# Optimization experiments

Hardware: AMD Instinct MI355X
Metric: run time of the kernel (lower is better)

## Reference

```python
import jax, jax.numpy as jnp
import numpy as np

B, N, D_V, D_MODEL, D_FF, N_HEADS = 32, 64, 6, 128, 512, 8


def _ln(x, g, b):
    m = x.mean(-1, keepdims=True)
    v = ((x - m) ** 2).mean(-1, keepdims=True)
    return (x - m) / jnp.sqrt(v + 1e-5) * g + b


def _mha(q_in, k_in, v_in, mask, Wq, Wk, Wv, Wo):
    # mask: (b, Lq, Lk) bool, True = attend
    b, Lq, D = q_in.shape
    H, dh = N_HEADS, D_MODEL // N_HEADS
    q = (q_in @ Wq).reshape(b, Lq, H, dh)
    k = (k_in @ Wk).reshape(b, k_in.shape[1], H, dh)
    v = (v_in @ Wv).reshape(b, v_in.shape[1], H, dh)
    s = jnp.einsum('bqhd,bkhd->bhqk', q, k) / (dh ** 0.5)
    s = jnp.where(mask[:, None, :, :], s, -1e9)
    o = jnp.einsum('bhqk,bkhd->bqhd', jax.nn.softmax(s, axis=-1), v).reshape(b, Lq, D)
    return o @ Wo


def setup_inputs() -> dict:
    key = jax.random.key(0)
    ks = jax.random.split(key, 40)
    def p(i, shape, scale=0.05):
        return jax.random.normal(ks[i], shape, dtype=jnp.float32) * scale
    nm = jax.random.randint(ks[1], (B, N, N), 0, 2, dtype=jnp.int32)
    nm = nm.at[:, jnp.arange(N), jnp.arange(N)].set(1)  # self always a neighbor
    inp = {
        'agent_infos': jax.random.normal(ks[0], (B, N, N, D_V), dtype=jnp.float32),
        'neighbor_masks': nm,
        'padding_mask': jnp.ones((B, N), dtype=jnp.int32),
        'is_from_my_env': jnp.ones((B,), dtype=jnp.int32),
        # src_embed
        'W_emb': p(2, (D_V, D_MODEL)), 'b_emb': jnp.zeros((D_MODEL,), jnp.float32),
        # encoder layer (self-attn + FFN, post-LN)
        'Wq': p(3, (D_MODEL, D_MODEL)), 'Wk': p(4, (D_MODEL, D_MODEL)),
        'Wv': p(5, (D_MODEL, D_MODEL)), 'Wo': p(6, (D_MODEL, D_MODEL)),
        'ln1_g': jnp.ones((D_MODEL,), jnp.float32), 'ln1_b': jnp.zeros((D_MODEL,), jnp.float32),
        'W1': p(7, (D_MODEL, D_FF)), 'b1': jnp.zeros((D_FF,), jnp.float32),
        'W2': p(8, (D_FF, D_MODEL)), 'b2': jnp.zeros((D_MODEL,), jnp.float32),
        'ln2_g': jnp.ones((D_MODEL,), jnp.float32), 'ln2_b': jnp.zeros((D_MODEL,), jnp.float32),
        # decoder layer (cross-attn + FFN, post-LN)
        'Uq': p(9, (D_MODEL, D_MODEL)), 'Uk': p(10, (D_MODEL, D_MODEL)),
        'Uv': p(11, (D_MODEL, D_MODEL)), 'Uo': p(12, (D_MODEL, D_MODEL)),
        'ln3_g': jnp.ones((D_MODEL,), jnp.float32), 'ln3_b': jnp.zeros((D_MODEL,), jnp.float32),
        'W3': p(13, (D_MODEL, D_FF)), 'b3': jnp.zeros((D_FF,), jnp.float32),
        'W4': p(14, (D_FF, D_MODEL)), 'b4': jnp.zeros((D_MODEL,), jnp.float32),
        'ln4_g': jnp.ones((D_MODEL,), jnp.float32), 'ln4_b': jnp.zeros((D_MODEL,), jnp.float32),
        # generator (single-head query/key scorer)
        'Wg_q': p(15, (D_MODEL, D_MODEL)), 'Wg_k': p(16, (D_MODEL, D_MODEL)),
    }
    return inp


def reference(agent_infos, neighbor_masks, padding_mask, is_from_my_env,
              W_emb, b_emb, Wq, Wk, Wv, Wo, ln1_g, ln1_b, W1, b1, W2, b2, ln2_g, ln2_b,
              Uq, Uk, Uv, Uo, ln3_g, ln3_b, W3, b3, W4, b4, ln4_g, ln4_b, Wg_q, Wg_k):
    # Fold the per-agent python loop of the original into the batch dim: BN = B * N.
    src = agent_infos.reshape(B * N, N, D_V)
    neigh = neighbor_masks.reshape(B * N, N) != 0           # True = neighbor (attendable)
    x = src @ W_emb + b_emb                                 # (BN, N, D)
    src_mask = neigh[:, :, None] & neigh[:, None, :]        # (BN, N, N)
    x = _ln(x + _mha(x, x, x, src_mask, Wq, Wk, Wv, Wo), ln1_g, ln1_b)
    x = _ln(x + (jax.nn.relu(x @ W1 + b1) @ W2 + b2), ln2_g, ln2_b)
    # context vector -- faithful to the original get_context_vector (which sums rows
    # where pad_tokens==True, i.e. NON-neighbors, and divides by the neighbor count)
    pad = (~neigh)[:, :, None].astype(x.dtype)
    cnt = neigh.sum(axis=1).reshape(-1, 1, 1).astype(x.dtype)
    h_c = (x * pad).sum(axis=1, keepdims=True) / cnt        # (BN, 1, D)
    stm = neigh[:, None, :]                                 # src_tgt_mask (BN, 1, N)
    y = _ln(h_c + _mha(h_c, x, x, stm, Uq, Uk, Uv, Uo), ln3_g, ln3_b)
    y = _ln(y + (jax.nn.relu(y @ W3 + b3) @ W4 + b4), ln4_g, ln4_b)
    logits = jnp.einsum('bqd,bkd->bqk', y @ Wg_q, x @ Wg_k) / (D_MODEL ** 0.5)
    probs = jnp.where(stm, jax.nn.sigmoid(logits), 0.0)[:, 0, :]   # (BN, N)
    att_scores = probs.reshape(B, N, N)
    num_agents = padding_mask.sum(axis=1).astype(x.dtype).reshape(B, 1, 1)
    avg_h_c_N = h_c.reshape(B, N, D_MODEL).sum(axis=1, keepdims=True) / num_agents
    return att_scores, avg_h_c_N
```

## Files before the change

### kernel.cpp

```cpp
#include <hip/hip_runtime.h>
#include <hip/hip_bf16.h>
#include <math.h>

#define ITEMS 2048
#define SEQ   64
#define DM    128
#define DFF   512
#define ATT_OFF 131072

typedef unsigned short u16;
typedef __attribute__((ext_vector_type(4))) unsigned short ushort4v;
typedef __attribute__((ext_vector_type(8))) short short8v;
typedef __attribute__((ext_vector_type(4))) float float4v;

#define MFMA16(a,b,c) __builtin_amdgcn_mfma_f32_16x16x32_bf16(a,b,c,0,0,0)

#define XST 136
#define OST 136
#define QST 56
#define PST 76
#define VST 72

#define XS_B   0
#define OB_B   17408
#define QH_B   34816
#define KH_B   41984
#define VT_B   49152
#define P_B    34816
#define WALL_B 34816
#define SALL_B 38912
#define PALL_B 40960
#define TALL_B 43008
#define FF_B   38912
#define W4P_B  40960
#define HC_B   17408
#define QV_B   17920
#define OV_B   18432
#define YV_B   18944
#define Y2_B   19456
#define GW_B   19968
#define NF_B   51456
#define PF_B   51712
#define CNT_B  51968
#define NA_B   51972
#define NB_B   51976
#define ARENA_SZ 51984

__device__ __forceinline__ u16 f2b(float f){
  union { float f; unsigned u; } v; v.f = f;
  unsigned r = (v.u + 0x7fffu + ((v.u >> 16) & 1u)) >> 16;
  return (u16)r;
}
__device__ __forceinline__ float b2f(u16 h){
  union { unsigned u; float f; } v; v.u = ((unsigned)h) << 16;
  return v.f;
}
__device__ __forceinline__ float wsum(float v){
  #pragma unroll
  for (int off = 1; off < 64; off <<= 1) v += __shfl_xor(v, off);
  return v;
}
__device__ __forceinline__ void ln_vec(float* v, const float* g, const float* b, int lane){
  float v0 = v[lane], v1 = v[lane+64];
  float m  = wsum(v0+v1) * (1.f/128.f);
  float d0 = v0-m, d1 = v1-m;
  float var = wsum(d0*d0+d1*d1) * (1.f/128.f);
  float inv = rsqrtf(var + 1e-5f);
  v[lane]    = d0*inv*g[lane]    + b[lane];
  v[lane+64] = d1*inv*g[lane+64] + b[lane+64];
}

__global__ void prep_all(const float* __restrict__ Wq, const float* __restrict__ Wk,
                         const float* __restrict__ Wv, const float* __restrict__ Wo,
                         const float* __restrict__ Uk, const float* __restrict__ Uv,
                         const float* __restrict__ W1, const float* __restrict__ W2,
                         u16* __restrict__ wts){
  int idx = blockIdx.x*256 + threadIdx.x;
  if (idx >= 229376) return;
  if (idx < 98304){
    int wsel = idx >> 14, r = idx & 16383;
    const float* tab[6] = {Wq,Wk,Wv,Wo,Uk,Uv};
    int o = r >> 7, i = r & 127;
    wts[idx] = f2b(tab[wsel][i*128 + o]);
  } else if (idx < 163840){
    int r = idx - 98304;
    int o = r >> 7, i = r & 127;
    wts[idx] = f2b(W1[i*512 + o]);
  } else {
    int r = idx - 163840;
    int o = r >> 9, i = r & 511;
    wts[idx] = f2b(W2[i*128 + o]);
  }
}

__global__ void init_avg(float* __restrict__ out){
  out[ATT_OFF + blockIdx.x*256 + threadIdx.x] = 0.f;
}

__global__ __launch_bounds__(256, 3) void vicsek_fused(
    const float* __restrict__ agent_infos,
    const int*   __restrict__ nmask,
    const int*   __restrict__ pmask,
    const u16*   __restrict__ wts,
    const float* __restrict__ W_emb, const float* __restrict__ b_emb,
    const float* __restrict__ ln1g,  const float* __restrict__ ln1b,
    const float* __restrict__ b1,    const float* __restrict__ b2,
    const float* __restrict__ ln2g,  const float* __restrict__ ln2b,
    const float* __restrict__ Uq,    const float* __restrict__ Uo,
    const float* __restrict__ ln3g,  const float* __restrict__ ln3b,
    const float* __restrict__ W3,    const float* __restrict__ b3,
    const float* __restrict__ W4,    const float* __restrict__ b4,
    const float* __restrict__ ln4g,  const float* __restrict__ ln4b,
    const float* __restrict__ Wgq,   const float* __restrict__ Wgk,
    float* __restrict__ out)
{
  __shared__ __align__(16) char arena[ARENA_SZ];
  u16* Xs = (u16*)(arena + XS_B);
  u16* Ob = (u16*)(arena + OB_B);
  u16* Qh = (u16*)(arena + QH_B);
  u16* Kh = (u16*)(arena + KH_B);
  u16* VT = (u16*)(arena + VT_B);
  u16* Pl = (u16*)(arena + P_B);
  float* neighf = (float*)(arena + NF_B);
  float* padf   = (float*)(arena + PF_B);
  float* cnt_s  = (float*)(arena + CNT_B);
  float* na_s   = (float*)(arena + NA_B);
  unsigned long long* nb_s = (unsigned long long*)(arena + NB_B);

  const int item = blockIdx.x;
  const int tid  = threadIdx.x;
  const int lane = tid & 63;
  const int w    = tid >> 6;
  const int row0 = w*16;
  const int arow = lane & 15;
  const int akg  = lane >> 4;

  const u16* WqT = wts;          const u16* WkT = wts + 16384;
  const u16* WvT = wts + 32768;  const u16* WoT = wts + 49152;
  const u16* UkT = wts + 65536;  const u16* UvT = wts + 81920;
  const u16* W1T = wts + 98304;  const u16* W2T = wts + 163840;

  if (w == 0){
    int m = nmask[item*SEQ + lane];
    neighf[lane] = m ? 1.f : 0.f;
    padf[lane]   = m ? 0.f : 1.f;
    float c = wsum(m ? 1.f : 0.f);
    unsigned long long bb = __ballot(m != 0);
    if (lane == 0){ cnt_s[0] = c; nb_s[0] = bb; }
  }
  if (w == 1){
    float na = wsum((float)pmask[(item>>6)*SEQ + lane]);
    if (lane == 0) na_s[0] = na;
  }

  const float* src = agent_infos + (size_t)item*SEQ*6;
  for (int e = tid; e < SEQ*DM; e += 256){
    int r = e >> 7, c = e & 127;
    float a = b_emb[c];
    #pragma unroll
    for (int k = 0; k < 6; k++) a += src[r*6+k]*W_emb[k*DM+c];
    Xs[r*XST + c] = f2b(a);
  }
  __syncthreads();

  const unsigned long long nbits = nb_s[0];

  short8v aX[4];
  #pragma unroll
  for (int k = 0; k < 4; k++) aX[k] = *(const short8v*)(Xs + (row0+arow)*XST + k*32 + akg*8);

  for (int h = 0; h < 8; h++){
    __syncthreads();
    for (int idx = tid; idx < 1024; idx += 256){
      int r = idx >> 4, c2 = idx & 15;
      Qh[r*QST + 16 + c2] = 0;
      Kh[r*QST + 16 + c2] = 0;
    }
    {
      const u16* wq = WqT + (h*16+arow)*128 + akg*8;
      const u16* wk = WkT + (h*16+arow)*128 + akg*8;
      const u16* wv = WvT + (h*16+arow)*128 + akg*8;
      float4v cq = {0,0,0,0}, ck = {0,0,0,0}, cv = {0,0,0,0};
      #pragma unroll
      for (int k = 0; k < 4; k++){
        short8v bqf = *(const short8v*)(wq + k*32);
        short8v bkf = *(const short8v*)(wk + k*32);
        short8v bvf = *(const short8v*)(wv + k*32);
        cq = MFMA16(aX[k], bqf, cq);
        ck = MFMA16(aX[k], bkf, ck);
        cv = MFMA16(bvf, aX[k], cv);
      }
      #pragma unroll
      for (int i = 0; i < 4; i++){
        Qh[(row0+akg*4+i)*QST + arow] = f2b(cq[i]);
        Kh[(row0+akg*4+i)*QST + arow] = f2b(ck[i]);
        VT[(akg*4+i)*VST + row0 + arow] = f2b(cv[i]);
      }
    }
    __syncthreads();
    short8v bq = *(const short8v*)(Qh + (row0+arow)*QST + akg*8);
    float4v st[4];
    #pragma unroll
    for (int kb = 0; kb < 4; kb++){
      short8v akf = *(const short8v*)(Kh + (kb*16+arow)*QST + akg*8);
      float4v z = {0,0,0,0};
      st[kb] = MFMA16(akf, bq, z);
    }
    bool qok = (nbits >> (row0+arow)) & 1ull;
    float pr[16]; float mx = -3.0e38f;
    #pragma unroll
    for (int kb = 0; kb < 4; kb++)
      #pragma unroll
      for (int i = 0; i < 4; i++){
        int key = kb*16 + akg*4 + i;
        float s = st[kb][i]*0.25f;
        if (!qok || !((nbits>>key)&1ull)) s = -1.0e9f;
        pr[kb*4+i] = s; mx = fmaxf(mx, s);
      }
    mx = fmaxf(mx, __shfl_xor(mx,16)); mx = fmaxf(mx, __shfl_xor(mx,32));
    float sum = 0.f;
    #pragma unroll
    for (int z = 0; z < 16; z++){ pr[z] = __expf(pr[z]-mx); sum += pr[z]; }
    sum += __shfl_xor(sum,16); sum += __shfl_xor(sum,32);
    float inv = 1.f/sum;
    #pragma unroll
    for (int kb = 0; kb < 4; kb++)
      #pragma unroll
      for (int i = 0; i < 4; i++)
        Pl[(kb*16+akg*4+i)*PST + row0 + arow] = f2b(pr[kb*4+i]*inv);
    float4v ot = {0,0,0,0};
    #pragma unroll
    for (int c2 = 0; c2 < 2; c2++){
      short8v avf = *(const short8v*)(VT + arow*VST + c2*32 + akg*8);
      short8v bp;
      #pragma unroll
      for (int j = 0; j < 8; j++) bp[j] = (short)Pl[(c2*32+akg*8+j)*PST + row0 + arow];
      ot = MFMA16(avf, bp, ot);
    }
    ushort4v ov4;
    #pragma unroll
    for (int i = 0; i < 4; i++) ov4[i] = f2b(ot[i]);
    *(ushort4v*)(Ob + (row0+arow)*OST + h*16 + akg*4) = ov4;
  }

  {
    float4v accW[8];
    #pragma unroll
    for (int t = 0; t < 8; t++)
      #pragma unroll
      for (int i = 0; i < 4; i++)
        accW[t][i] = b2f(Xs[(row0+akg*4+i)*XST + t*16 + arow]);
    short8v aO[4];
    #pragma unroll
    for (int k = 0; k < 4; k++) aO[k] = *(const short8v*)(Ob + (row0+arow)*OST + k*32 + akg*8);
    #pragma unroll
    for (int k = 0; k < 4; k++)
      #pragma unroll
      for (int t = 0; t < 8; t++)
        accW[t] = MFMA16(aO[k], *(const short8v*)(WoT + (t*16+arow)*128 + k*32 + akg*8), accW[t]);
    float g8[8], bb8[8];
    #pragma unroll
    for (int t = 0; t < 8; t++){ g8[t] = ln1g[t*16+arow]; bb8[t] = ln1b[t*16+arow]; }
    #pragma unroll
    for (int i = 0; i < 4; i++){
      float sm = 0.f;
      #pragma unroll
      for (int t = 0; t < 8; t++) sm += accW[t][i];
      sm += __shfl_xor(sm,1); sm += __shfl_xor(sm,2); sm += __shfl_xor(sm,4); sm += __shfl_xor(sm,8);
      float mean = sm*(1.f/128.f);
      float vs = 0.f;
      #pragma unroll
      for (int t = 0; t < 8; t++){ float d = accW[t][i]-mean; vs += d*d; }
      vs += __shfl_xor(vs,1); vs += __shfl_xor(vs,2); vs += __shfl_xor(vs,4); vs += __shfl_xor(vs,8);
      float inv = rsqrtf(vs*(1.f/128.f) + 1e-5f);
      #pragma unroll
      for (int t = 0; t < 8; t++)
        Xs[(row0+akg*4+i)*XST + t*16 + arow] = f2b((accW[t][i]-mean)*inv*g8[t] + bb8[t]);
    }
  }
  #pragma unroll
  for (int k = 0; k < 4; k++) aX[k] = *(const short8v*)(Xs + (row0+arow)*XST + k*32 + akg*8);

  {
    float4v accY[8];
    #pragma unroll
    for (int t = 0; t < 8; t++){
      float bb = b2[t*16 + arow];
      #pragma unroll
      for (int i = 0; i < 4; i++)
        accY[t][i] = bb + b2f(Xs[(row0+akg*4+i)*XST + t*16 + arow]);
    }
    for (int c = 0; c < 4; c++){
      #pragma unroll
      for (int t = 0; t < 8; t++){
        float bb = b1[c*128 + t*16 + arow];
        float4v acc = {bb,bb,bb,bb};
        #pragma unroll
        for (int k = 0; k < 4; k++)
          acc = MFMA16(aX[k], *(const short8v*)(W1T + (c*128+t*16+arow)*128 + k*32 + akg*8), acc);
        #pragma unroll
        for (int i = 0; i < 4; i++)
          Ob[(row0+akg*4+i)*OST + t*16 + arow] = f2b(fmaxf(acc[i], 0.f));
      }
      #pragma unroll
      for (int k = 0; k < 4; k++){
        short8v aH = *(const short8v*)(Ob + (row0+arow)*OST + k*32 + akg*8);
        #pragma unroll
        for (int t = 0; t < 8; t++)
          accY[t] = MFMA16(aH, *(const short8v*)(W2T + (t*16+arow)*512 + c*128 + k*32 + akg*8), accY[t]);
      }
    }
    float g8[8], bb8[8];
    #pragma unroll
    for (int t = 0; t < 8; t++){ g8[t] = ln2g[t*16+arow]; bb8[t] = ln2b[t*16+arow]; }
    #pragma unroll
    for (int i = 0; i < 4; i++){
      float sm = 0.f;
      #pragma unroll
      for (int t = 0; t < 8; t++) sm += accY[t][i];
      sm += __shfl_xor(sm,1); sm += __shfl_xor(sm,2); sm += __shfl_xor(sm,4); sm += __shfl_xor(sm,8);
      float mean = sm*(1.f/128.f);
      float vs = 0.f;
      #pragma unroll
      for (int t = 0; t < 8; t++){ float d = accY[t][i]-mean; vs += d*d; }
      vs += __shfl_xor(vs,1); vs += __shfl_xor(vs,2); vs += __shfl_xor(vs,4); vs += __shfl_xor(vs,8);
      float inv = rsqrtf(vs*(1.f/128.f) + 1e-5f);
      #pragma unroll
      for (int t = 0; t < 8; t++)
        Xs[(row0+akg*4+i)*XST + t*16 + arow] = f2b((accY[t][i]-mean)*inv*g8[t] + bb8[t]);
    }
  }
  __syncthreads();

  float* hc   = (float*)(arena + HC_B);
  float* qv   = (float*)(arena + QV_B);
  float* ov   = (float*)(arena + OV_B);
  float* yv   = (float*)(arena + YV_B);
  float* y2   = (float*)(arena + Y2_B);
  float* gw   = (float*)(arena + GW_B);
  float* wall = (float*)(arena + WALL_B);
  float* sall = (float*)(arena + SALL_B);
  float* pall = (float*)(arena + PALL_B);
  float* tall = (float*)(arena + TALL_B);
  float* ff   = (float*)(arena + FF_B);
  float* w4p  = (float*)(arena + W4P_B);

  if (tid < DM){
    float a = 0.f;
    for (int r = 0; r < SEQ; r++) a += b2f(Xs[r*XST + tid]) * padf[r];
    a /= cnt_s[0];
    hc[tid] = a;
    atomicAdd(&out[ATT_OFF + (item>>6)*DM + tid], a/na_s[0]);
  }
  __syncthreads();

  if (tid < DM){
    float a = 0.f;
    #pragma unroll 8
    for (int e = 0; e < DM; e++) a += hc[e]*Uq[e*DM + tid];
    qv[tid] = a;
  }
  __syncthreads();
  if (tid < DM){
    #pragma unroll
    for (int h = 0; h < 8; h++){
      float a = 0.f;
      #pragma unroll
      for (int d = 0; d < 16; d++) a += b2f(UkT[(h*16+d)*128 + tid]) * qv[h*16+d];
      wall[h*128 + tid] = a;
    }
  }
  __syncthreads();
  for (int idx = tid; idx < 512; idx += 256){
    int h = idx >> 6, j = idx & 63;
    const short8v* xr = (const short8v*)(Xs + j*XST);
    const float* wv_ = wall + h*128;
    float a = 0.f;
    #pragma unroll
    for (int c8 = 0; c8 < 16; c8++){
      short8v v = xr[c8];
      #pragma unroll
      for (int q = 0; q < 8; q++) a += b2f((u16)v[q]) * wv_[c8*8+q];
    }
    sall[idx] = a*0.25f;
  }
  __syncthreads();
  for (int hh = w; hh < 8; hh += 4){
    float s = sall[hh*64 + lane];
    if (!((nbits>>lane)&1ull)) s = -1.0e9f;
    float mxx = s;
    #pragma unroll
    for (int off = 1; off < 64; off <<= 1) mxx = fmaxf(mxx, __shfl_xor(mxx, off));
    float p = __expf(s - mxx);
    float su = wsum(p);
    pall[hh*64 + lane] = p/su;
  }
  __syncthreads();
  for (int idx = tid; idx < 1024; idx += 256){
    int h = idx >> 7, c = idx & 127;
    float a = 0.f;
    for (int j = 0; j < SEQ; j++) a += pall[h*64+j] * b2f(Xs[j*XST + c]);
    tall[idx] = a;
  }
  __syncthreads();
  if (tid < DM){
    const short8v* ur = (const short8v*)(UvT + tid*128);
    const float* th = tall + (tid>>4)*128;
    float a = 0.f;
    #pragma unroll
    for (int c8 = 0; c8 < 16; c8++){
      short8v v = ur[c8];
      #pragma unroll
      for (int q = 0; q < 8; q++) a += b2f((u16)v[q]) * th[c8*8+q];
    }
    ov[tid] = a;
  }
  __syncthreads();
  if (tid < DM){
    float a = 0.f;
    #pragma unroll 8
    for (int e = 0; e < DM; e++) a += ov[e]*Uo[e*DM + tid];
    yv[tid] = hc[tid] + a;
  }
  __syncthreads();
  if (w == 0) ln_vec(yv, ln3g, ln3b, lane);
  __syncthreads();

  for (int j = tid; j < DFF; j += 256){
    float a = b3[j];
    #pragma unroll 8
    for (int e = 0; e < DM; e++) a += yv[e]*W3[e*DFF + j];
    ff[j] = fmaxf(a, 0.f);
  }
  __syncthreads();
  {
    int o = tid & 127, half = tid >> 7;
    float a = 0.f;
    #pragma unroll 8
    for (int j = half*256; j < half*256+256; j++) a += ff[j]*W4[j*DM + o];
    w4p[tid] = a;
  }
  __syncthreads();
  if (tid < DM) y2[tid] = b4[tid] + yv[tid] + w4p[tid] + w4p[tid+128];
  __syncthreads();
  if (w == 0) ln_vec(y2, ln4g, ln4b, lane);
  __syncthreads();

  if (tid < DM){
    float a = 0.f;
    #pragma unroll 8
    for (int e = 0; e < DM; e++) a += y2[e]*Wgq[e*DM + tid];
    qv[tid] = a;
  }
  __syncthreads();
  if (tid < DM){
    const float4* wr = (const float4*)(Wgk + tid*DM);
    float a = 0.f;
    #pragma unroll
    for (int c4 = 0; c4 < 32; c4++){
      float4 v = wr[c4];
      a += v.x*qv[c4*4] + v.y*qv[c4*4+1] + v.z*qv[c4*4+2] + v.w*qv[c4*4+3];
    }
    gw[tid] = a;
  }
  __syncthreads();
  if (tid < SEQ){
    const short8v* xr = (const short8v*)(Xs + tid*XST);
    float a = 0.f;
    #pragma unroll
    for (int c8 = 0; c8 < 16; c8++){
      short8v v = xr[c8];
      #pragma unroll
      for (int q = 0; q < 8; q++) a += b2f((u16)v[q]) * gw[c8*8+q];
    }
    a *= 0.08838834764831845f;
    out[(size_t)item*SEQ + tid] = ((nbits>>tid)&1ull) ? (1.f/(1.f+__expf(-a))) : 0.f;
  }
}

extern "C" void kernel_launch(void* const* d_in, const int* in_sizes, int n_in,
                              void* d_out, int out_size, void* d_ws, size_t ws_size,
                              hipStream_t stream)
{
  const float* agent_infos = (const float*)d_in[0];
  const int*   nmask       = (const int*)  d_in[1];
  const int*   pmask       = (const int*)  d_in[2];
  const float* W_emb = (const float*)d_in[4];
  const float* b_emb = (const float*)d_in[5];
  const float* Wq    = (const float*)d_in[6];
  const float* Wk    = (const float*)d_in[7];
  const float* Wv    = (const float*)d_in[8];
  const float* Wo    = (const float*)d_in[9];
  const float* ln1g  = (const float*)d_in[10];
  const float* ln1b  = (const float*)d_in[11];
  const float* W1    = (const float*)d_in[12];
  const float* b1    = (const float*)d_in[13];
  const float* W2    = (const float*)d_in[14];
  const float* b2    = (const float*)d_in[15];
  const float* ln2g  = (const float*)d_in[16];
  const float* ln2b  = (const float*)d_in[17];
  const float* Uq    = (const float*)d_in[18];
  const float* Uk    = (const float*)d_in[19];
  const float* Uv    = (const float*)d_in[20];
  const float* Uo    = (const float*)d_in[21];
  const float* ln3g  = (const float*)d_in[22];
  const float* ln3b  = (const float*)d_in[23];
  const float* W3    = (const float*)d_in[24];
  const float* b3    = (const float*)d_in[25];
  const float* W4    = (const float*)d_in[26];
  const float* b4    = (const float*)d_in[27];
  const float* ln4g  = (const float*)d_in[28];
  const float* ln4b  = (const float*)d_in[29];
  const float* Wgq   = (const float*)d_in[30];
  const float* Wgk   = (const float*)d_in[31];

  float* out = (float*)d_out;
  u16*   wts = (u16*)d_ws;

  prep_all<<<896, 256, 0, stream>>>(Wq, Wk, Wv, Wo, Uk, Uv, W1, W2, wts);
  init_avg<<<16, 256, 0, stream>>>(out);
  vicsek_fused<<<ITEMS, 256, 0, stream>>>(
      agent_infos, nmask, pmask, wts, W_emb, b_emb,
      ln1g, ln1b, b1, b2, ln2g, ln2b, Uq, Uo, ln3g, ln3b,
      W3, b3, W4, b4, ln4g, ln4b, Wgq, Wgk, out);
}
```

Measured before the change: 652.7 us.

## Precompute all-head QKV once, drop per-head syncs, and use bf16 transposed decoder weights

```diff
diff --git a/kernel.cpp b/kernel.cpp
--- a/kernel.cpp
+++ b/kernel.cpp
@@ -16,35 +16,49 @@
 #define MFMA16(a,b,c) __builtin_amdgcn_mfma_f32_16x16x32_bf16(a,b,c,0,0,0)
 
 #define XST 136
-#define OST 136
-#define QST 56
+#define VST 72
 #define PST 76
-#define VST 72
 
 #define XS_B   0
-#define OB_B   17408
-#define QH_B   34816
-#define KH_B   41984
-#define VT_B   49152
-#define P_B    34816
-#define WALL_B 34816
-#define SALL_B 38912
-#define PALL_B 40960
-#define TALL_B 43008
-#define FF_B   38912
-#define W4P_B  40960
-#define HC_B   17408
-#define QV_B   17920
-#define OV_B   18432
-#define YV_B   18944
-#define Y2_B   19456
-#define GW_B   19968
-#define NF_B   51456
-#define PF_B   51712
-#define CNT_B  51968
-#define NA_B   51972
-#define NB_B   51976
-#define ARENA_SZ 51984
+#define QS_B   17408
+#define KS_B   34816
+#define VT_B   52224
+#define PL_B   70656
+#define ZB_B   80384
+#define PF_B   80400
+#define CNT_B  80656
+#define NA_B   80660
+#define NB_B   80664
+#define ARENA_SZ 80672
+
+#define HC_B   (KS_B+0)
+#define QV_B   (KS_B+512)
+#define OV_B   (KS_B+1024)
+#define YV_B   (KS_B+1536)
+#define Y2_B   (KS_B+2048)
+#define GW_B   (KS_B+2560)
+#define WALL_B (VT_B+0)
+#define SALL_B (VT_B+4096)
+#define PALL_B (VT_B+6144)
+#define TALL_B (VT_B+8192)
+#define FF_B   (VT_B+12288)
+#define W4P_B  (VT_B+14336)
+
+#define WQ_O   0
+#define WK_O   16384
+#define WV_O   32768
+#define WO_O   49152
+#define UK_O   65536
+#define UV_O   81920
+#define W1_O   98304
+#define W2_O   163840
+#define UQ_O   229376
+#define UO_O   245760
+#define WGQ_O  262144
+#define WGK_O  278528
+#define W3_O   294912
+#define W4_O   360448
+#define WS_TOT 425984
 
 __device__ __forceinline__ u16 f2b(float f){
   union { float f; unsigned u; } v; v.f = f;
@@ -69,35 +83,66 @@
   v[lane]    = d0*inv*g[lane]    + b[lane];
   v[lane+64] = d1*inv*g[lane+64] + b[lane+64];
 }
+__device__ __forceinline__ float dot128(const u16* __restrict__ wrow, const float* __restrict__ x){
+  const short8v* wr = (const short8v*)wrow;
+  float a = 0.f;
+  #pragma unroll
+  for (int c8 = 0; c8 < 16; c8++){
+    short8v v = wr[c8];
+    #pragma unroll
+    for (int q = 0; q < 8; q++) a += b2f((u16)v[q]) * x[c8*8+q];
+  }
+  return a;
+}
 
 __global__ void prep_all(const float* __restrict__ Wq, const float* __restrict__ Wk,
                          const float* __restrict__ Wv, const float* __restrict__ Wo,
                          const float* __restrict__ Uk, const float* __restrict__ Uv,
                          const float* __restrict__ W1, const float* __restrict__ W2,
+                         const float* __restrict__ Uq, const float* __restrict__ Uo,
+                         const float* __restrict__ Wgq, const float* __restrict__ Wgk,
+                         const float* __restrict__ W3, const float* __restrict__ W4,
                          u16* __restrict__ wts){
   int idx = blockIdx.x*256 + threadIdx.x;
-  if (idx >= 229376) return;
+  if (idx >= WS_TOT) return;
+  float v;
   if (idx < 98304){
     int wsel = idx >> 14, r = idx & 16383;
     const float* tab[6] = {Wq,Wk,Wv,Wo,Uk,Uv};
     int o = r >> 7, i = r & 127;
-    wts[idx] = f2b(tab[wsel][i*128 + o]);
-  } else if (idx < 163840){
-    int r = idx - 98304;
-    int o = r >> 7, i = r & 127;
-    wts[idx] = f2b(W1[i*512 + o]);
+    v = tab[wsel][i*128 + o];
+  } else if (idx < W2_O){
+    int r = idx - W1_O; int o = r >> 7, i = r & 127;
+    v = W1[i*512 + o];
+  } else if (idx < UQ_O){
+    int r = idx - W2_O; int o = r >> 9, i = r & 511;
+    v = W2[i*128 + o];
+  } else if (idx < UO_O){
+    int r = idx - UQ_O; int o = r >> 7, i = r & 127;
+    v = Uq[i*128 + o];
+  } else if (idx < WGQ_O){
+    int r = idx - UO_O; int o = r >> 7, i = r & 127;
+    v = Uo[i*128 + o];
+  } else if (idx < WGK_O){
+    int r = idx - WGQ_O; int o = r >> 7, i = r & 127;
+    v = Wgq[i*128 + o];
+  } else if (idx < W3_O){
+    v = Wgk[idx - WGK_O];
+  } else if (idx < W4_O){
+    int r = idx - W3_O; int j = r >> 7, e = r & 127;
+    v = W3[e*512 + j];
   } else {
-    int r = idx - 163840;
-    int o = r >> 9, i = r & 511;
-    wts[idx] = f2b(W2[i*128 + o]);
-  }
+    int r = idx - W4_O; int o = r >> 9, j = r & 511;
+    v = W4[j*128 + o];
+  }
+  wts[idx] = f2b(v);
 }
 
 __global__ void init_avg(float* __restrict__ out){
   out[ATT_OFF + blockIdx.x*256 + threadIdx.x] = 0.f;
 }
 
-__global__ __launch_bounds__(256, 3) void vicsek_fused(
+__global__ __launch_bounds__(256, 2) void vicsek_fused(
     const float* __restrict__ agent_infos,
     const int*   __restrict__ nmask,
     const int*   __restrict__ pmask,
@@ -106,25 +151,21 @@
     const float* __restrict__ ln1g,  const float* __restrict__ ln1b,
     const float* __restrict__ b1,    const float* __restrict__ b2,
     const float* __restrict__ ln2g,  const float* __restrict__ ln2b,
-    const float* __restrict__ Uq,    const float* __restrict__ Uo,
     const float* __restrict__ ln3g,  const float* __restrict__ ln3b,
-    const float* __restrict__ W3,    const float* __restrict__ b3,
-    const float* __restrict__ W4,    const float* __restrict__ b4,
+    const float* __restrict__ b3,    const float* __restrict__ b4,
     const float* __restrict__ ln4g,  const float* __restrict__ ln4b,
-    const float* __restrict__ Wgq,   const float* __restrict__ Wgk,
     float* __restrict__ out)
 {
   __shared__ __align__(16) char arena[ARENA_SZ];
   u16* Xs = (u16*)(arena + XS_B);
-  u16* Ob = (u16*)(arena + OB_B);
-  u16* Qh = (u16*)(arena + QH_B);
-  u16* Kh = (u16*)(arena + KH_B);
+  u16* Qs = (u16*)(arena + QS_B);
+  u16* Ks = (u16*)(arena + KS_B);
   u16* VT = (u16*)(arena + VT_B);
-  u16* Pl = (u16*)(arena + P_B);
-  float* neighf = (float*)(arena + NF_B);
-  float* padf   = (float*)(arena + PF_B);
-  float* cnt_s  = (float*)(arena + CNT_B);
-  float* na_s   = (float*)(arena + NA_B);
+  u16* Pl = (u16*)(arena + PL_B);
+  u16* zb = (u16*)(arena + ZB_B);
+  float* padf  = (float*)(arena + PF_B);
+  float* cnt_s = (float*)(arena + CNT_B);
+  float* na_s  = (float*)(arena + NA_B);
   unsigned long long* nb_s = (unsigned long long*)(arena + NB_B);
 
   const int item = blockIdx.x;
@@ -135,15 +176,17 @@
   const int arow = lane & 15;
   const int akg  = lane >> 4;
 
-  const u16* WqT = wts;          const u16* WkT = wts + 16384;
-  const u16* WvT = wts + 32768;  const u16* WoT = wts + 49152;
-  const u16* UkT = wts + 65536;  const u16* UvT = wts + 81920;
-  const u16* W1T = wts + 98304;  const u16* W2T = wts + 163840;
+  const u16* WqT = wts + WQ_O;  const u16* WkT = wts + WK_O;
+  const u16* WvT = wts + WV_O;  const u16* WoT = wts + WO_O;
+  const u16* UkT = wts + UK_O;  const u16* UvT = wts + UV_O;
+  const u16* W1T = wts + W1_O;  const u16* W2T = wts + W2_O;
+  const u16* UqT = wts + UQ_O;  const u16* UoT = wts + UO_O;
+  const u16* WgqT = wts + WGQ_O; const u16* WgkB = wts + WGK_O;
+  const u16* W3T = wts + W3_O;  const u16* W4T = wts + W4_O;
 
   if (w == 0){
     int m = nmask[item*SEQ + lane];
-    neighf[lane] = m ? 1.f : 0.f;
-    padf[lane]   = m ? 0.f : 1.f;
+    padf[lane] = m ? 0.f : 1.f;
     float c = wsum(m ? 1.f : 0.f);
     unsigned long long bb = __ballot(m != 0);
     if (lane == 0){ cnt_s[0] = c; nb_s[0] = bb; }
@@ -152,6 +195,7 @@
     float na = wsum((float)pmask[(item>>6)*SEQ + lane]);
     if (lane == 0) na_s[0] = na;
   }
+  if (tid < 8) zb[tid] = 0;
 
   const float* src = agent_infos + (size_t)item*SEQ*6;
   for (int e = tid; e < SEQ*DM; e += 256){
@@ -169,42 +213,41 @@
   #pragma unroll
   for (int k = 0; k < 4; k++) aX[k] = *(const short8v*)(Xs + (row0+arow)*XST + k*32 + akg*8);
 
+  for (int t = 0; t < 8; t++){
+    const u16* wq = WqT + (t*16+arow)*128 + akg*8;
+    const u16* wk = WkT + (t*16+arow)*128 + akg*8;
+    const u16* wv = WvT + (t*16+arow)*128 + akg*8;
+    float4v cq = {0,0,0,0}, ck = {0,0,0,0}, cv = {0,0,0,0};
+    #pragma unroll
+    for (int k = 0; k < 4; k++){
+      cq = MFMA16(aX[k], *(const short8v*)(wq + k*32), cq);
+      ck = MFMA16(aX[k], *(const short8v*)(wk + k*32), ck);
+      cv = MFMA16(*(const short8v*)(wv + k*32), aX[k], cv);
+    }
+    #pragma unroll
+    for (int i = 0; i < 4; i++){
+      Qs[(row0+akg*4+i)*XST + t*16+arow] = f2b(cq[i]);
+      Ks[(row0+akg*4+i)*XST + t*16+arow] = f2b(ck[i]);
+      VT[(t*16+akg*4+i)*VST + row0+arow] = f2b(cv[i]);
+    }
+  }
+  float4v accW[8];
+  #pragma unroll
+  for (int t = 0; t < 8; t++)
+    #pragma unroll
+    for (int i = 0; i < 4; i++)
+      accW[t][i] = b2f(Xs[(row0+akg*4+i)*XST + t*16 + arow]);
+  __syncthreads();
+
   for (int h = 0; h < 8; h++){
-    __syncthreads();
-    for (int idx = tid; idx < 1024; idx += 256){
-      int r = idx >> 4, c2 = idx & 15;
-      Qh[r*QST + 16 + c2] = 0;
-      Kh[r*QST + 16 + c2] = 0;
-    }
-    {
-      const u16* wq = WqT + (h*16+arow)*128 + akg*8;
-      const u16* wk = WkT + (h*16+arow)*128 + akg*8;
-      const u16* wv = WvT + (h*16+arow)*128 + akg*8;
-      float4v cq = {0,0,0,0}, ck = {0,0,0,0}, cv = {0,0,0,0};
-      #pragma unroll
-      for (int k = 0; k < 4; k++){
-        short8v bqf = *(const short8v*)(wq + k*32);
-        short8v bkf = *(const short8v*)(wk + k*32);
-        short8v bvf = *(const short8v*)(wv + k*32);
-        cq = MFMA16(aX[k], bqf, cq);
-        ck = MFMA16(aX[k], bkf, ck);
-        cv = MFMA16(bvf, aX[k], cv);
-      }
-      #pragma unroll
-      for (int i = 0; i < 4; i++){
-        Qh[(row0+akg*4+i)*QST + arow] = f2b(cq[i]);
-        Kh[(row0+akg*4+i)*QST + arow] = f2b(ck[i]);
-        VT[(akg*4+i)*VST + row0 + arow] = f2b(cv[i]);
-      }
-    }
-    __syncthreads();
-    short8v bq = *(const short8v*)(Qh + (row0+arow)*QST + akg*8);
+    const u16* qp = (akg < 2) ? (Qs + (row0+arow)*XST + h*16 + akg*8) : zb;
+    short8v bq = *(const short8v*)qp;
     float4v st[4];
     #pragma unroll
     for (int kb = 0; kb < 4; kb++){
-      short8v akf = *(const short8v*)(Kh + (kb*16+arow)*QST + akg*8);
+      const u16* kp = (akg < 2) ? (Ks + (kb*16+arow)*XST + h*16 + akg*8) : zb;
       float4v z = {0,0,0,0};
-      st[kb] = MFMA16(akf, bq, z);
+      st[kb] = MFMA16(*(const short8v*)kp, bq, z);
     }
     bool qok = (nbits >> (row0+arow)) & 1ull;
     float pr[16]; float mx = -3.0e38f;
@@ -227,32 +270,26 @@
     for (int kb = 0; kb < 4; kb++)
       #pragma unroll
       for (int i = 0; i < 4; i++)
-        Pl[(kb*16+akg*4+i)*PST + row0 + arow] = f2b(pr[kb*4+i]*inv);
+        Pl[(kb*16+akg*4+i)*PST + row0+arow] = f2b(pr[kb*4+i]*inv);
     float4v ot = {0,0,0,0};
     #pragma unroll
     for (int c2 = 0; c2 < 2; c2++){
-      short8v avf = *(const short8v*)(VT + arow*VST + c2*32 + akg*8);
+      short8v av = *(const short8v*)(VT + (h*16+arow)*VST + c2*32 + akg*8);
       short8v bp;
       #pragma unroll
-      for (int j = 0; j < 8; j++) bp[j] = (short)Pl[(c2*32+akg*8+j)*PST + row0 + arow];
-      ot = MFMA16(avf, bp, ot);
+      for (int j = 0; j < 8; j++) bp[j] = (short)Pl[(c2*32+akg*8+j)*PST + row0+arow];
+      ot = MFMA16(av, bp, ot);
     }
     ushort4v ov4;
     #pragma unroll
     for (int i = 0; i < 4; i++) ov4[i] = f2b(ot[i]);
-    *(ushort4v*)(Ob + (row0+arow)*OST + h*16 + akg*4) = ov4;
+    *(ushort4v*)(Xs + (row0+arow)*XST + h*16 + akg*4) = ov4;
   }
 
   {
-    float4v accW[8];
-    #pragma unroll
-    for (int t = 0; t < 8; t++)
-      #pragma unroll
-      for (int i = 0; i < 4; i++)
-        accW[t][i] = b2f(Xs[(row0+akg*4+i)*XST + t*16 + arow]);
     short8v aO[4];
     #pragma unroll
-    for (int k = 0; k < 4; k++) aO[k] = *(const short8v*)(Ob + (row0+arow)*OST + k*32 + akg*8);
+    for (int k = 0; k < 4; k++) aO[k] = *(const short8v*)(Xs + (row0+arow)*XST + k*32 + akg*8);
     #pragma unroll
     for (int k = 0; k < 4; k++)
       #pragma unroll
@@ -282,6 +319,7 @@
   for (int k = 0; k < 4; k++) aX[k] = *(const short8v*)(Xs + (row0+arow)*XST + k*32 + akg*8);
 
   {
+    u16* Hb = Qs;
     float4v accY[8];
     #pragma unroll
     for (int t = 0; t < 8; t++){
@@ -300,11 +338,11 @@
           acc = MFMA16(aX[k], *(const short8v*)(W1T + (c*128+t*16+arow)*128 + k*32 + akg*8), acc);
         #pragma unroll
         for (int i = 0; i < 4; i++)
-          Ob[(row0+akg*4+i)*OST + t*16 + arow] = f2b(fmaxf(acc[i], 0.f));
+          Hb[(row0+akg*4+i)*XST + t*16 + arow] = f2b(fmaxf(acc[i], 0.f));
       }
       #pragma unroll
       for (int k = 0; k < 4; k++){
-        short8v aH = *(const short8v*)(Ob + (row0+arow)*OST + k*32 + akg*8);
+        short8v aH = *(const short8v*)(Hb + (row0+arow)*XST + k*32 + akg*8);
         #pragma unroll
         for (int t = 0; t < 8; t++)
           accY[t] = MFMA16(aH, *(const short8v*)(W2T + (t*16+arow)*512 + c*128 + k*32 + akg*8), accY[t]);
@@ -347,6 +385,7 @@
 
   if (tid < DM){
     float a = 0.f;
+    #pragma unroll 8
     for (int r = 0; r < SEQ; r++) a += b2f(Xs[r*XST + tid]) * padf[r];
     a /= cnt_s[0];
     hc[tid] = a;
@@ -354,12 +393,7 @@
   }
   __syncthreads();
 
-  if (tid < DM){
-    float a = 0.f;
-    #pragma unroll 8
-    for (int e = 0; e < DM; e++) a += hc[e]*Uq[e*DM + tid];
-    qv[tid] = a;
-  }
+  if (tid < DM) qv[tid] = dot128(UqT + tid*128, hc);
   __syncthreads();
   if (tid < DM){
     #pragma unroll
@@ -396,48 +430,47 @@
     pall[hh*64 + lane] = p/su;
   }
   __syncthreads();
-  for (int idx = tid; idx < 1024; idx += 256){
-    int h = idx >> 7, c = idx & 127;
-    float a = 0.f;
-    for (int j = 0; j < SEQ; j++) a += pall[h*64+j] * b2f(Xs[j*XST + c]);
-    tall[idx] = a;
-  }
-  __syncthreads();
-  if (tid < DM){
-    const short8v* ur = (const short8v*)(UvT + tid*128);
-    const float* th = tall + (tid>>4)*128;
-    float a = 0.f;
-    #pragma unroll
-    for (int c8 = 0; c8 < 16; c8++){
-      short8v v = ur[c8];
-      #pragma unroll
-      for (int q = 0; q < 8; q++) a += b2f((u16)v[q]) * th[c8*8+q];
-    }
-    ov[tid] = a;
-  }
-  __syncthreads();
-  if (tid < DM){
-    float a = 0.f;
-    #pragma unroll 8
-    for (int e = 0; e < DM; e++) a += ov[e]*Uo[e*DM + tid];
-    yv[tid] = hc[tid] + a;
-  }
+  {
+    int task = tid >> 1, jh = tid & 1;
+    int h = task >> 4, c8 = task & 15;
+    float acc8[8] = {0,0,0,0,0,0,0,0};
+    #pragma unroll 4
+    for (int jj = 0; jj < 32; jj++){
+      int j = jh*32 + jj;
+      short8v v = *(const short8v*)(Xs + j*XST + c8*8);
+      float pj = pall[h*64 + j];
+      #pragma unroll
+      for (int q = 0; q < 8; q++) acc8[q] += pj * b2f((u16)v[q]);
+    }
+    #pragma unroll
+    for (int q = 0; q < 8; q++) acc8[q] += __shfl_xor(acc8[q], 1);
+    if (jh == 0){
+      #pragma unroll
+      for (int q = 0; q < 8; q++) tall[h*128 + c8*8 + q] = acc8[q];
+    }
+  }
+  __syncthreads();
+  if (tid < DM) ov[tid] = dot128(UvT + tid*128, tall + (tid>>4)*128);
+  __syncthreads();
+  if (tid < DM) yv[tid] = hc[tid] + dot128(UoT + tid*128, ov);
   __syncthreads();
   if (w == 0) ln_vec(yv, ln3g, ln3b, lane);
   __syncthreads();
 
-  for (int j = tid; j < DFF; j += 256){
-    float a = b3[j];
-    #pragma unroll 8
-    for (int e = 0; e < DM; e++) a += yv[e]*W3[e*DFF + j];
-    ff[j] = fmaxf(a, 0.f);
-  }
+  for (int j = tid; j < DFF; j += 256)
+    ff[j] = fmaxf(b3[j] + dot128(W3T + j*128, yv), 0.f);
   __syncthreads();
   {
     int o = tid & 127, half = tid >> 7;
+    const short8v* wr = (const short8v*)(W4T + o*512 + half*256);
+    const float* fh = ff + half*256;
     float a = 0.f;
-    #pragma unroll 8
-    for (int j = half*256; j < half*256+256; j++) a += ff[j]*W4[j*DM + o];
+    #pragma unroll
+    for (int c8 = 0; c8 < 32; c8++){
+      short8v v = wr[c8];
+      #pragma unroll
+      for (int q = 0; q < 8; q++) a += b2f((u16)v[q]) * fh[c8*8+q];
+    }
     w4p[tid] = a;
   }
   __syncthreads();
@@ -446,33 +479,12 @@
   if (w == 0) ln_vec(y2, ln4g, ln4b, lane);
   __syncthreads();
 
-  if (tid < DM){
-    float a = 0.f;
-    #pragma unroll 8
-    for (int e = 0; e < DM; e++) a += y2[e]*Wgq[e*DM + tid];
-    qv[tid] = a;
-  }
-  __syncthreads();
-  if (tid < DM){
-    const float4* wr = (const float4*)(Wgk + tid*DM);
-    float a = 0.f;
-    #pragma unroll
-    for (int c4 = 0; c4 < 32; c4++){
-      float4 v = wr[c4];
-      a += v.x*qv[c4*4] + v.y*qv[c4*4+1] + v.z*qv[c4*4+2] + v.w*qv[c4*4+3];
-    }
-    gw[tid] = a;
-  }
+  if (tid < DM) qv[tid] = dot128(WgqT + tid*128, y2);
+  __syncthreads();
+  if (tid < DM) gw[tid] = dot128(WgkB + tid*128, qv);
   __syncthreads();
   if (tid < SEQ){
-    const short8v* xr = (const short8v*)(Xs + tid*XST);
-    float a = 0.f;
-    #pragma unroll
-    for (int c8 = 0; c8 < 16; c8++){
-      short8v v = xr[c8];
-      #pragma unroll
-      for (int q = 0; q < 8; q++) a += b2f((u16)v[q]) * gw[c8*8+q];
-    }
+    float a = dot128(Xs + tid*XST, gw) ;
     a *= 0.08838834764831845f;
     out[(size_t)item*SEQ + tid] = ((nbits>>tid)&1ull) ? (1.f/(1.f+__expf(-a))) : 0.f;
   }
@@ -517,10 +529,11 @@
   float* out = (float*)d_out;
   u16*   wts = (u16*)d_ws;
 
-  prep_all<<<896, 256, 0, stream>>>(Wq, Wk, Wv, Wo, Uk, Uv, W1, W2, wts);
+  prep_all<<<(WS_TOT+255)/256, 256, 0, stream>>>(Wq, Wk, Wv, Wo, Uk, Uv, W1, W2,
+                                                 Uq, Uo, Wgq, Wgk, W3, W4, wts);
   init_avg<<<16, 256, 0, stream>>>(out);
   vicsek_fused<<<ITEMS, 256, 0, stream>>>(
       agent_infos, nmask, pmask, wts, W_emb, b_emb,
-      ln1g, ln1b, b1, b2, ln2g, ln2b, Uq, Uo, ln3g, ln3b,
-      W3, b3, W4, b4, ln4g, ln4b, Wgq, Wgk, out);
-}
+      ln1g, ln1b, b1, b2, ln2g, ln2b, ln3g, ln3b,
+      b3, b4, ln4g, ln4b, out);
+}
```

After: 636.1 us. 1.03x faster.
